# Kernel optimization log

Measured on AMD Instinct MI355X. Metric: run time of the kernel, lower is better.

Reference implementation:

```python
import jax, jax.numpy as jnp
import numpy as np
from jax import lax

NUM_CLASSES = 5  # config['training']['num_classes_per_task']
EMBED_DIM = 64


def _conv(x, w, b, pad):
    y = lax.conv_general_dilated(x, w, (1, 1), [(pad, pad), (pad, pad)],
                                 dimension_numbers=('NCHW', 'OIHW', 'NCHW'))
    return y + b[None, :, None, None]


def _maxpool2(x):
    n, c, h, w = x.shape
    return x.reshape(n, c, h // 2, 2, w // 2, 2).max(axis=(3, 5))


def _lenet(x, c1w, c1b, c2w, c2b, f1w, f1b, f2w, f2b, f3w, f3b):
    h = _maxpool2(jax.nn.relu(_conv(x, c1w, c1b, pad=2)))   # [N,6,14,14]
    h = _maxpool2(jax.nn.relu(_conv(h, c2w, c2b, pad=0)))   # [N,16,5,5]
    h = h.reshape(h.shape[0], -1)                            # [N,400]
    h = jax.nn.relu(h @ f1w.T + f1b)                         # [N,120]
    h = jax.nn.relu(h @ f2w.T + f2b)                         # [N,84]
    return h @ f3w.T + f3b                                   # [N,64]


def setup_inputs() -> dict:
    key = jax.random.key(0)
    ks = jax.random.split(key, 12)
    s = 0.1
    return {
        'x': jax.random.normal(ks[0], (20480, 1, 28, 28), dtype=jnp.float32),
        'c1w': jax.random.normal(ks[1], (6, 1, 5, 5), dtype=jnp.float32) * s,
        'c1b': jnp.zeros((6,), dtype=jnp.float32),
        'c2w': jax.random.normal(ks[2], (16, 6, 5, 5), dtype=jnp.float32) * s,
        'c2b': jnp.zeros((16,), dtype=jnp.float32),
        'f1w': jax.random.normal(ks[3], (120, 400), dtype=jnp.float32) * s,
        'f1b': jnp.zeros((120,), dtype=jnp.float32),
        'f2w': jax.random.normal(ks[4], (84, 120), dtype=jnp.float32) * s,
        'f2b': jnp.zeros((84,), dtype=jnp.float32),
        'f3w': jax.random.normal(ks[5], (EMBED_DIM, 84), dtype=jnp.float32) * s,
        'f3b': jnp.zeros((EMBED_DIM,), dtype=jnp.float32),
    }


def reference(x, c1w, c1b, c2w, c2b, f1w, f1b, f2w, f2b, f3w, f3b):
    emb = _lenet(x, c1w, c1b, c2w, c2b, f1w, f1b, f2w, f2b, f3w, f3b)  # [N,D]
    # Source builds a flat prototypes list of all N*D scalars / num_classes,
    # but only indices 0..D-1 are ever read -> first embedding row / num_classes.
    proto = emb[0] / NUM_CLASSES                     # [D]
    s = jax.nn.softmax(emb, axis=1)                  # softmax over dim 1
    # fun_L(x, p) = sqrt((x-p)^2) = |x-p|
    logits = jnp.abs(s - proto[None, :])             # [N,D]
    batch_size = x.shape[0] // NUM_CLASSES
    return logits.reshape(batch_size, NUM_CLASSES, -1)
```

## Files before the change

kernel.cpp:

```cpp
#include <hip/hip_runtime.h>


__device__ __forceinline__ int xcd_swizzle(int orig, int nwg) {
    int xcd = orig & 7, q = nwg >> 3, r = nwg & 7;
    int base = (xcd < r) ? xcd * (q + 1) : r * (q + 1) + (xcd - r) * q;
    return base + (orig >> 3);
}

__global__ __launch_bounds__(256) void transpose_x(
    const float* __restrict__ x, float* __restrict__ xt, int nc)
{
    __shared__ float t[64][65];
    const int tx = threadIdx.x & 63, ty = threadIdx.x >> 6;
    const int p0 = blockIdx.x * 64, n0 = blockIdx.y * 64;
    #pragma unroll
    for (int rr = 0; rr < 16; ++rr) {
        int nl = rr * 4 + ty;
        int pp = p0 + tx;
        int pr = pp >> 5, pc = pp & 31;
        float v = 0.f;
        if (pr >= 2 && pr < 30 && pc >= 2 && pc < 30)
            v = x[(size_t)(n0 + nl) * 784 + (pr - 2) * 28 + (pc - 2)];
        t[tx][nl] = v;
    }
    __syncthreads();
    #pragma unroll
    for (int rr = 0; rr < 16; ++rr) {
        int pl = rr * 4 + ty;
        xt[(size_t)(p0 + pl) * nc + n0 + tx] = t[pl][tx];
    }
}

__global__ __launch_bounds__(256, 4) void conv1_bt(
    const float* __restrict__ xt, const float* __restrict__ c1w,
    const float* __restrict__ c1b, float* __restrict__ p1t, int nc)
{
    const int newid = xcd_swizzle(blockIdx.x, gridDim.x);
    const int grp = newid / 196, pos = newid - grp * 196;
    const int py = pos / 14, px = pos - py * 14;
    const int ia = grp * 512 + threadIdx.x;
    const int ib = ia + 256;
    const int pbase = (2 * py) * 32 + 2 * px;

    float pa[36], pb[36];
    #pragma unroll
    for (int r = 0; r < 6; ++r)
        #pragma unroll
        for (int cc = 0; cc < 6; ++cc) {
            const float* p = &xt[(size_t)(pbase + r * 32 + cc) * nc];
            pa[r * 6 + cc] = p[ia];
            pb[r * 6 + cc] = p[ib];
        }

    #pragma unroll
    for (int ch = 0; ch < 6; ++ch) {
        float w[25];
        const float* wp = c1w + ch * 25;
        #pragma unroll
        for (int k = 0; k < 25; ++k) w[k] = wp[k];
        float b = c1b[ch];
        float ma = -1e30f, mb = -1e30f;
        #pragma unroll
        for (int dy = 0; dy < 2; ++dy)
        #pragma unroll
        for (int dx = 0; dx < 2; ++dx) {
            float aa = b, ab = b;
            #pragma unroll
            for (int ky = 0; ky < 5; ++ky)
            #pragma unroll
            for (int kx = 0; kx < 5; ++kx) {
                float ww = w[ky * 5 + kx];
                aa += pa[(dy + ky) * 6 + dx + kx] * ww;
                ab += pb[(dy + ky) * 6 + dx + kx] * ww;
            }
            ma = fmaxf(ma, aa); mb = fmaxf(mb, ab);
        }
        float* o = &p1t[(size_t)(ch * 196 + pos) * nc];
        o[ia] = fmaxf(ma, 0.f);
        o[ib] = fmaxf(mb, 0.f);
    }
}

__global__ __launch_bounds__(256, 4) void conv2_bt(
    const float* __restrict__ p1t, const float* __restrict__ c2w,
    const float* __restrict__ c2b, float* __restrict__ ht, int nc)
{
    const int newid = xcd_swizzle(blockIdx.x, gridDim.x);
    const int grp = newid / 25, pos = newid - grp * 25;
    const int qy = pos / 5, qx = pos - qy * 5;
    const int img = grp * 256 + threadIdx.x;
    const int y0 = 2 * qy, x0 = 2 * qx;

    float acc[64];
    #pragma unroll
    for (int i = 0; i < 64; ++i) acc[i] = 0.f;

    #pragma unroll 1
    for (int ci = 0; ci < 6; ++ci) {
        float pa[36];
        #pragma unroll
        for (int r = 0; r < 6; ++r)
            #pragma unroll
            for (int cc = 0; cc < 6; ++cc)
                pa[r * 6 + cc] =
                    p1t[(size_t)(ci * 196 + (y0 + r) * 14 + x0 + cc) * nc + img];
        #pragma unroll
        for (int oc = 0; oc < 16; ++oc) {
            float w[25];
            const float* wp = c2w + (oc * 6 + ci) * 25;
            #pragma unroll
            for (int k = 0; k < 25; ++k) w[k] = wp[k];
            #pragma unroll
            for (int ky = 0; ky < 5; ++ky)
            #pragma unroll
            for (int kx = 0; kx < 5; ++kx) {
                float ww = w[ky * 5 + kx];
                acc[oc*4+0] += pa[ky*6+kx]       * ww;
                acc[oc*4+1] += pa[ky*6+kx+1]     * ww;
                acc[oc*4+2] += pa[(ky+1)*6+kx]   * ww;
                acc[oc*4+3] += pa[(ky+1)*6+kx+1] * ww;
            }
        }
    }
    #pragma unroll
    for (int oc = 0; oc < 16; ++oc) {
        float b = c2b[oc];
        float m = fmaxf(fmaxf(acc[oc*4+0], acc[oc*4+1]),
                        fmaxf(acc[oc*4+2], acc[oc*4+3])) + b;
        ht[(size_t)(oc * 25 + pos) * nc + img] = fmaxf(m, 0.f);
    }
}

__global__ __launch_bounds__(256, 2) void lenet_fc_t(
    const float* __restrict__ ht,
    const float* __restrict__ f1w, const float* __restrict__ f1b,
    const float* __restrict__ f2w, const float* __restrict__ f2b,
    const float* __restrict__ f3w, const float* __restrict__ f3b,
    float* __restrict__ emb, int nc)
{
    __shared__ float wpool[6400];
    __shared__ float a1[32 * 121];
    __shared__ float a2[32 * 85];

    const int tid = threadIdx.x;
    const int n0 = blockIdx.x * 32;
    const int ig = tid & 7;
    const int og = tid >> 3;

    float acc[16];
    #pragma unroll
    for (int j = 0; j < 16; ++j) acc[j] = 0.f;

    for (int kc = 0; kc < 400; kc += 50) {
        __syncthreads();
        for (int i = tid; i < 6000; i += 256) {
            int r = i / 50, c = i - r * 50;
            int rg = r >> 2, rl = r & 3;
            wpool[c * 128 + (((rg ^ (c & 7)) << 2) | rl)] = f1w[r * 400 + kc + c];
        }
        __syncthreads();
        if (og < 30) {
            #pragma unroll 2
            for (int kk = 0; kk < 50; ++kk) {
                const float* hp = &ht[(size_t)(kc + kk) * nc + n0 + ig * 4];
                float h0 = hp[0], h1 = hp[1], h2 = hp[2], h3 = hp[3];
                float4 wv = *(const float4*)&wpool[kk * 128 + ((og ^ (kk & 7)) << 2)];
                acc[0]  += h0 * wv.x; acc[1]  += h0 * wv.y;
                acc[2]  += h0 * wv.z; acc[3]  += h0 * wv.w;
                acc[4]  += h1 * wv.x; acc[5]  += h1 * wv.y;
                acc[6]  += h1 * wv.z; acc[7]  += h1 * wv.w;
                acc[8]  += h2 * wv.x; acc[9]  += h2 * wv.y;
                acc[10] += h2 * wv.z; acc[11] += h2 * wv.w;
                acc[12] += h3 * wv.x; acc[13] += h3 * wv.y;
                acc[14] += h3 * wv.z; acc[15] += h3 * wv.w;
            }
        }
    }
    __syncthreads();
    if (og < 30) {
        #pragma unroll
        for (int j = 0; j < 4; ++j) {
            int o = og * 4 + j;
            float bb = f1b[o];
            a1[(ig * 4 + 0) * 121 + o] = fmaxf(acc[j]      + bb, 0.f);
            a1[(ig * 4 + 1) * 121 + o] = fmaxf(acc[4 + j]  + bb, 0.f);
            a1[(ig * 4 + 2) * 121 + o] = fmaxf(acc[8 + j]  + bb, 0.f);
            a1[(ig * 4 + 3) * 121 + o] = fmaxf(acc[12 + j] + bb, 0.f);
        }
    }
    #pragma unroll
    for (int j = 0; j < 16; ++j) acc[j] = 0.f;

    for (int kc = 0; kc < 120; kc += 60) {
        __syncthreads();
        for (int i = tid; i < 84 * 60; i += 256) {
            int r = i / 60, c = i - r * 60;
            wpool[r * 61 + c] = f2w[r * 120 + kc + c];
        }
        __syncthreads();
        if (og < 21) {
            for (int kk = 0; kk < 60; ++kk) {
                float h0 = a1[(ig * 4 + 0) * 121 + kc + kk];
                float h1 = a1[(ig * 4 + 1) * 121 + kc + kk];
                float h2 = a1[(ig * 4 + 2) * 121 + kc + kk];
                float h3 = a1[(ig * 4 + 3) * 121 + kc + kk];
                #pragma unroll
                for (int j = 0; j < 4; ++j) {
                    float w = wpool[(og * 4 + j) * 61 + kk];
                    acc[j]      += h0 * w;
                    acc[4 + j]  += h1 * w;
                    acc[8 + j]  += h2 * w;
                    acc[12 + j] += h3 * w;
                }
            }
        }
    }
    __syncthreads();
    if (og < 21) {
        #pragma unroll
        for (int j = 0; j < 4; ++j) {
            int o = og * 4 + j;
            float bb = f2b[o];
            a2[(ig * 4 + 0) * 85 + o] = fmaxf(acc[j]      + bb, 0.f);
            a2[(ig * 4 + 1) * 85 + o] = fmaxf(acc[4 + j]  + bb, 0.f);
            a2[(ig * 4 + 2) * 85 + o] = fmaxf(acc[8 + j]  + bb, 0.f);
            a2[(ig * 4 + 3) * 85 + o] = fmaxf(acc[12 + j] + bb, 0.f);
        }
    }
    for (int i = tid; i < 64 * 84; i += 256) {
        int r = i / 84, c = i - r * 84;
        wpool[r * 85 + c] = f3w[i];
    }
    #pragma unroll
    for (int j = 0; j < 16; ++j) acc[j] = 0.f;
    __syncthreads();

    if (og < 16) {
        for (int kk = 0; kk < 84; ++kk) {
            float h0 = a2[(ig * 4 + 0) * 85 + kk];
            float h1 = a2[(ig * 4 + 1) * 85 + kk];
            float h2 = a2[(ig * 4 + 2) * 85 + kk];
            float h3 = a2[(ig * 4 + 3) * 85 + kk];
            #pragma unroll
            for (int j = 0; j < 4; ++j) {
                float w = wpool[(og * 4 + j) * 85 + kk];
                acc[j]      += h0 * w;
                acc[4 + j]  += h1 * w;
                acc[8 + j]  += h2 * w;
                acc[12 + j] += h3 * w;
            }
        }
    }
    __syncthreads();
    if (og < 16) {
        #pragma unroll
        for (int j = 0; j < 4; ++j) {
            int o = og * 4 + j;
            float bb = f3b[o];
            #pragma unroll
            for (int r = 0; r < 4; ++r)
                a1[(ig * 4 + r) * 67 + o] = acc[r * 4 + j] + bb;
        }
    }
    __syncthreads();
    for (int i = tid; i < 2048; i += 256) {
        int row = i >> 6, o = i & 63;
        emb[(size_t)(n0 + row) * 64 + o] = a1[row * 67 + o];
    }
}

__global__ __launch_bounds__(256) void proto_head(
    const float* __restrict__ emb, float* __restrict__ out, int N)
{
    int row  = blockIdx.x * 4 + (threadIdx.x >> 6);
    int lane = threadIdx.x & 63;
    if (row >= N) return;
    float v = emb[(size_t)row * 64 + lane];
    float m = v;
    #pragma unroll
    for (int off = 32; off >= 1; off >>= 1)
        m = fmaxf(m, __shfl_xor(m, off));
    float e = expf(v - m);
    float s = e;
    #pragma unroll
    for (int off = 32; off >= 1; off >>= 1)
        s += __shfl_xor(s, off);
    float sm = e / s;
    float proto = emb[lane] * 0.2f;
    out[(size_t)row * 64 + lane] = fabsf(sm - proto);
}

extern "C" void kernel_launch(void* const* d_in, const int* in_sizes, int n_in,
                              void* d_out, int out_size, void* d_ws, size_t ws_size,
                              hipStream_t stream)
{
    const float* x   = (const float*)d_in[0];
    const float* c1w = (const float*)d_in[1];
    const float* c1b = (const float*)d_in[2];
    const float* c2w = (const float*)d_in[3];
    const float* c2b = (const float*)d_in[4];
    const float* f1w = (const float*)d_in[5];
    const float* f1b = (const float*)d_in[6];
    const float* f2w = (const float*)d_in[7];
    const float* f2b = (const float*)d_in[8];
    const float* f3w = (const float*)d_in[9];
    const float* f3b = (const float*)d_in[10];
    float* out = (float*)d_out;

    const int N = in_sizes[0] / 784;
    float* base = (float*)d_ws;

    int c = 40;
    const int cands[] = {1, 2, 4, 5, 8, 10, 20, 40};
    for (int k = 0; k < 8; ++k) {
        int cd = cands[k];
        if (N % cd) continue;
        int ncq = N / cd;
        if (ncq % 512) continue;
        size_t need = (size_t)8800 * ncq + (size_t)256 * N;
        if (need <= ws_size) { c = cd; break; }
    }
    const int nc = N / c;

    float* xt  = base;
    float* p1t = base + (size_t)1024 * nc;
    float* ht_ = base;
    float* emb = base + (size_t)2200 * nc;

    for (int k = 0; k < c; ++k) {
        int n0 = k * nc;
        transpose_x<<<dim3(16, nc / 64), 256, 0, stream>>>(
            x + (size_t)n0 * 784, xt, nc);
        conv1_bt<<<196 * (nc / 512), 256, 0, stream>>>(
            xt, c1w, c1b, p1t, nc);
        conv2_bt<<<25 * (nc / 256), 256, 0, stream>>>(
            p1t, c2w, c2b, ht_, nc);
        lenet_fc_t<<<nc / 32, 256, 0, stream>>>(
            ht_, f1w, f1b, f2w, f2b, f3w, f3b, emb + (size_t)n0 * 64, nc);
    }
    proto_head<<<(N + 3) / 4, 256, 0, stream>>>(emb, out, N);
}
```

Measured before the change: 324.3 us.

## Split FC stack into transposed per-layer kernels and vectorize conv1 loads

Replaces the fused shared-memory FC kernel with three separate batch-transposed FC kernels (fc1/fc2/fc3). Each thread computes two images with float2 loads and reads weights as uniform scalar loads. Conv1 now uses float2 loads and stores of adjacent images, and conv2 splits its output channels into two passes to cut register pressure, with launch bounds relaxed. The proto head reads the transposed embedding, so each thread does a full-row softmax. In exchange, intermediates make extra global round-trips between kernels and more launches are issued.

```diff
diff --git a/kernel.cpp b/kernel.cpp
--- a/kernel.cpp
+++ b/kernel.cpp
@@ -31,26 +31,23 @@
     }
 }
 
-__global__ __launch_bounds__(256, 4) void conv1_bt(
+__global__ __launch_bounds__(256, 2) void conv1_bt(
     const float* __restrict__ xt, const float* __restrict__ c1w,
     const float* __restrict__ c1b, float* __restrict__ p1t, int nc)
 {
     const int newid = xcd_swizzle(blockIdx.x, gridDim.x);
     const int grp = newid / 196, pos = newid - grp * 196;
     const int py = pos / 14, px = pos - py * 14;
-    const int ia = grp * 512 + threadIdx.x;
-    const int ib = ia + 256;
+    const int img = grp * 512 + threadIdx.x * 2;
     const int pbase = (2 * py) * 32 + 2 * px;
 
-    float pa[36], pb[36];
+    float2 p[36];
     #pragma unroll
     for (int r = 0; r < 6; ++r)
         #pragma unroll
-        for (int cc = 0; cc < 6; ++cc) {
-            const float* p = &xt[(size_t)(pbase + r * 32 + cc) * nc];
-            pa[r * 6 + cc] = p[ia];
-            pb[r * 6 + cc] = p[ib];
-        }
+        for (int cc = 0; cc < 6; ++cc)
+            p[r * 6 + cc] =
+                *(const float2*)&xt[(size_t)(pbase + r * 32 + cc) * nc + img];
 
     #pragma unroll
     for (int ch = 0; ch < 6; ++ch) {
@@ -70,18 +67,18 @@
             #pragma unroll
             for (int kx = 0; kx < 5; ++kx) {
                 float ww = w[ky * 5 + kx];
-                aa += pa[(dy + ky) * 6 + dx + kx] * ww;
-                ab += pb[(dy + ky) * 6 + dx + kx] * ww;
+                float2 pv = p[(dy + ky) * 6 + dx + kx];
+                aa += pv.x * ww;
+                ab += pv.y * ww;
             }
             ma = fmaxf(ma, aa); mb = fmaxf(mb, ab);
         }
-        float* o = &p1t[(size_t)(ch * 196 + pos) * nc];
-        o[ia] = fmaxf(ma, 0.f);
-        o[ib] = fmaxf(mb, 0.f);
-    }
-}
-
-__global__ __launch_bounds__(256, 4) void conv2_bt(
+        float2 o2 = make_float2(fmaxf(ma, 0.f), fmaxf(mb, 0.f));
+        *(float2*)&p1t[(size_t)(ch * 196 + pos) * nc + img] = o2;
+    }
+}
+
+__global__ __launch_bounds__(256, 2) void conv2_bt(
     const float* __restrict__ p1t, const float* __restrict__ c2w,
     const float* __restrict__ c2b, float* __restrict__ ht, int nc)
 {
@@ -91,203 +88,176 @@
     const int img = grp * 256 + threadIdx.x;
     const int y0 = 2 * qy, x0 = 2 * qx;
 
-    float acc[64];
-    #pragma unroll
-    for (int i = 0; i < 64; ++i) acc[i] = 0.f;
-
     #pragma unroll 1
-    for (int ci = 0; ci < 6; ++ci) {
-        float pa[36];
-        #pragma unroll
-        for (int r = 0; r < 6; ++r)
+    for (int pass = 0; pass < 2; ++pass) {
+        float acc[32];
+        #pragma unroll
+        for (int i = 0; i < 32; ++i) acc[i] = 0.f;
+
+        #pragma unroll 1
+        for (int ci = 0; ci < 6; ++ci) {
+            float pa[36];
             #pragma unroll
-            for (int cc = 0; cc < 6; ++cc)
-                pa[r * 6 + cc] =
-                    p1t[(size_t)(ci * 196 + (y0 + r) * 14 + x0 + cc) * nc + img];
-        #pragma unroll
-        for (int oc = 0; oc < 16; ++oc) {
-            float w[25];
-            const float* wp = c2w + (oc * 6 + ci) * 25;
+            for (int r = 0; r < 6; ++r)
+                #pragma unroll
+                for (int cc = 0; cc < 6; ++cc)
+                    pa[r * 6 + cc] =
+                        p1t[(size_t)(ci * 196 + (y0 + r) * 14 + x0 + cc) * nc + img];
             #pragma unroll
-            for (int k = 0; k < 25; ++k) w[k] = wp[k];
-            #pragma unroll
-            for (int ky = 0; ky < 5; ++ky)
-            #pragma unroll
-            for (int kx = 0; kx < 5; ++kx) {
-                float ww = w[ky * 5 + kx];
-                acc[oc*4+0] += pa[ky*6+kx]       * ww;
-                acc[oc*4+1] += pa[ky*6+kx+1]     * ww;
-                acc[oc*4+2] += pa[(ky+1)*6+kx]   * ww;
-                acc[oc*4+3] += pa[(ky+1)*6+kx+1] * ww;
-            }
-        }
-    }
-    #pragma unroll
-    for (int oc = 0; oc < 16; ++oc) {
-        float b = c2b[oc];
-        float m = fmaxf(fmaxf(acc[oc*4+0], acc[oc*4+1]),
-                        fmaxf(acc[oc*4+2], acc[oc*4+3])) + b;
-        ht[(size_t)(oc * 25 + pos) * nc + img] = fmaxf(m, 0.f);
-    }
-}
-
-__global__ __launch_bounds__(256, 2) void lenet_fc_t(
-    const float* __restrict__ ht,
-    const float* __restrict__ f1w, const float* __restrict__ f1b,
-    const float* __restrict__ f2w, const float* __restrict__ f2b,
-    const float* __restrict__ f3w, const float* __restrict__ f3b,
-    float* __restrict__ emb, int nc)
-{
-    __shared__ float wpool[6400];
-    __shared__ float a1[32 * 121];
-    __shared__ float a2[32 * 85];
-
-    const int tid = threadIdx.x;
-    const int n0 = blockIdx.x * 32;
-    const int ig = tid & 7;
-    const int og = tid >> 3;
-
-    float acc[16];
-    #pragma unroll
-    for (int j = 0; j < 16; ++j) acc[j] = 0.f;
-
-    for (int kc = 0; kc < 400; kc += 50) {
-        __syncthreads();
-        for (int i = tid; i < 6000; i += 256) {
-            int r = i / 50, c = i - r * 50;
-            int rg = r >> 2, rl = r & 3;
-            wpool[c * 128 + (((rg ^ (c & 7)) << 2) | rl)] = f1w[r * 400 + kc + c];
-        }
-        __syncthreads();
-        if (og < 30) {
-            #pragma unroll 2
-            for (int kk = 0; kk < 50; ++kk) {
-                const float* hp = &ht[(size_t)(kc + kk) * nc + n0 + ig * 4];
-                float h0 = hp[0], h1 = hp[1], h2 = hp[2], h3 = hp[3];
-                float4 wv = *(const float4*)&wpool[kk * 128 + ((og ^ (kk & 7)) << 2)];
-                acc[0]  += h0 * wv.x; acc[1]  += h0 * wv.y;
-                acc[2]  += h0 * wv.z; acc[3]  += h0 * wv.w;
-                acc[4]  += h1 * wv.x; acc[5]  += h1 * wv.y;
-                acc[6]  += h1 * wv.z; acc[7]  += h1 * wv.w;
-                acc[8]  += h2 * wv.x; acc[9]  += h2 * wv.y;
-                acc[10] += h2 * wv.z; acc[11] += h2 * wv.w;
-                acc[12] += h3 * wv.x; acc[13] += h3 * wv.y;
-                acc[14] += h3 * wv.z; acc[15] += h3 * wv.w;
-            }
-        }
-    }
-    __syncthreads();
-    if (og < 30) {
-        #pragma unroll
-        for (int j = 0; j < 4; ++j) {
-            int o = og * 4 + j;
-            float bb = f1b[o];
-            a1[(ig * 4 + 0) * 121 + o] = fmaxf(acc[j]      + bb, 0.f);
-            a1[(ig * 4 + 1) * 121 + o] = fmaxf(acc[4 + j]  + bb, 0.f);
-            a1[(ig * 4 + 2) * 121 + o] = fmaxf(acc[8 + j]  + bb, 0.f);
-            a1[(ig * 4 + 3) * 121 + o] = fmaxf(acc[12 + j] + bb, 0.f);
-        }
-    }
-    #pragma unroll
-    for (int j = 0; j < 16; ++j) acc[j] = 0.f;
-
-    for (int kc = 0; kc < 120; kc += 60) {
-        __syncthreads();
-        for (int i = tid; i < 84 * 60; i += 256) {
-            int r = i / 60, c = i - r * 60;
-            wpool[r * 61 + c] = f2w[r * 120 + kc + c];
-        }
-        __syncthreads();
-        if (og < 21) {
-            for (int kk = 0; kk < 60; ++kk) {
-                float h0 = a1[(ig * 4 + 0) * 121 + kc + kk];
-                float h1 = a1[(ig * 4 + 1) * 121 + kc + kk];
-                float h2 = a1[(ig * 4 + 2) * 121 + kc + kk];
-                float h3 = a1[(ig * 4 + 3) * 121 + kc + kk];
+            for (int o8 = 0; o8 < 8; ++o8) {
+                float w[25];
+                const float* wp = c2w + ((pass * 8 + o8) * 6 + ci) * 25;
                 #pragma unroll
-                for (int j = 0; j < 4; ++j) {
-                    float w = wpool[(og * 4 + j) * 61 + kk];
-                    acc[j]      += h0 * w;
-                    acc[4 + j]  += h1 * w;
-                    acc[8 + j]  += h2 * w;
-                    acc[12 + j] += h3 * w;
+                for (int k = 0; k < 25; ++k) w[k] = wp[k];
+                #pragma unroll
+                for (int ky = 0; ky < 5; ++ky)
+                #pragma unroll
+                for (int kx = 0; kx < 5; ++kx) {
+                    float ww = w[ky * 5 + kx];
+                    acc[o8*4+0] += pa[ky*6+kx]       * ww;
+                    acc[o8*4+1] += pa[ky*6+kx+1]     * ww;
+                    acc[o8*4+2] += pa[(ky+1)*6+kx]   * ww;
+                    acc[o8*4+3] += pa[(ky+1)*6+kx+1] * ww;
                 }
             }
         }
-    }
-    __syncthreads();
-    if (og < 21) {
-        #pragma unroll
-        for (int j = 0; j < 4; ++j) {
-            int o = og * 4 + j;
-            float bb = f2b[o];
-            a2[(ig * 4 + 0) * 85 + o] = fmaxf(acc[j]      + bb, 0.f);
-            a2[(ig * 4 + 1) * 85 + o] = fmaxf(acc[4 + j]  + bb, 0.f);
-            a2[(ig * 4 + 2) * 85 + o] = fmaxf(acc[8 + j]  + bb, 0.f);
-            a2[(ig * 4 + 3) * 85 + o] = fmaxf(acc[12 + j] + bb, 0.f);
-        }
-    }
-    for (int i = tid; i < 64 * 84; i += 256) {
-        int r = i / 84, c = i - r * 84;
-        wpool[r * 85 + c] = f3w[i];
-    }
-    #pragma unroll
-    for (int j = 0; j < 16; ++j) acc[j] = 0.f;
-    __syncthreads();
-
-    if (og < 16) {
-        for (int kk = 0; kk < 84; ++kk) {
-            float h0 = a2[(ig * 4 + 0) * 85 + kk];
-            float h1 = a2[(ig * 4 + 1) * 85 + kk];
-            float h2 = a2[(ig * 4 + 2) * 85 + kk];
-            float h3 = a2[(ig * 4 + 3) * 85 + kk];
-            #pragma unroll
-            for (int j = 0; j < 4; ++j) {
-                float w = wpool[(og * 4 + j) * 85 + kk];
-                acc[j]      += h0 * w;
-                acc[4 + j]  += h1 * w;
-                acc[8 + j]  += h2 * w;
-                acc[12 + j] += h3 * w;
-            }
-        }
-    }
-    __syncthreads();
-    if (og < 16) {
-        #pragma unroll
-        for (int j = 0; j < 4; ++j) {
-            int o = og * 4 + j;
-            float bb = f3b[o];
-            #pragma unroll
-            for (int r = 0; r < 4; ++r)
-                a1[(ig * 4 + r) * 67 + o] = acc[r * 4 + j] + bb;
-        }
-    }
-    __syncthreads();
-    for (int i = tid; i < 2048; i += 256) {
-        int row = i >> 6, o = i & 63;
-        emb[(size_t)(n0 + row) * 64 + o] = a1[row * 67 + o];
-    }
-}
-
-__global__ __launch_bounds__(256) void proto_head(
-    const float* __restrict__ emb, float* __restrict__ out, int N)
-{
-    int row  = blockIdx.x * 4 + (threadIdx.x >> 6);
-    int lane = threadIdx.x & 63;
-    if (row >= N) return;
-    float v = emb[(size_t)row * 64 + lane];
-    float m = v;
-    #pragma unroll
-    for (int off = 32; off >= 1; off >>= 1)
-        m = fmaxf(m, __shfl_xor(m, off));
-    float e = expf(v - m);
-    float s = e;
-    #pragma unroll
-    for (int off = 32; off >= 1; off >>= 1)
-        s += __shfl_xor(s, off);
-    float sm = e / s;
-    float proto = emb[lane] * 0.2f;
-    out[(size_t)row * 64 + lane] = fabsf(sm - proto);
+        #pragma unroll
+        for (int o8 = 0; o8 < 8; ++o8) {
+            int oc = pass * 8 + o8;
+            float b = c2b[oc];
+            float m = fmaxf(fmaxf(acc[o8*4+0], acc[o8*4+1]),
+                            fmaxf(acc[o8*4+2], acc[o8*4+3])) + b;
+            ht[(size_t)(oc * 25 + pos) * nc + img] = fmaxf(m, 0.f);
+        }
+    }
+}
+
+__global__ __launch_bounds__(256) void fc1_bt(
+    const float* __restrict__ ht, const float* __restrict__ f1w,
+    const float* __restrict__ f1b, float* __restrict__ a1t, int nc)
+{
+    const int newid = xcd_swizzle(blockIdx.x, gridDim.x);
+    const int grp = newid / 15, og = newid - grp * 15;
+    const int img = grp * 512 + threadIdx.x * 2;
+    const float* wb = f1w + og * 8 * 400;
+
+    float2 acc[8];
+    #pragma unroll
+    for (int j = 0; j < 8; ++j) acc[j] = make_float2(0.f, 0.f);
+
+    #pragma unroll 4
+    for (int k = 0; k < 400; ++k) {
+        float2 hv = *(const float2*)&ht[(size_t)k * nc + img];
+        #pragma unroll
+        for (int j = 0; j < 8; ++j) {
+            float w = wb[j * 400 + k];
+            acc[j].x += hv.x * w;
+            acc[j].y += hv.y * w;
+        }
+    }
+    #pragma unroll
+    for (int j = 0; j < 8; ++j) {
+        int o = og * 8 + j;
+        float b = f1b[o];
+        float2 o2 = make_float2(fmaxf(acc[j].x + b, 0.f),
+                                fmaxf(acc[j].y + b, 0.f));
+        *(float2*)&a1t[(size_t)o * nc + img] = o2;
+    }
+}
+
+__global__ __launch_bounds__(256) void fc2_bt(
+    const float* __restrict__ a1t, const float* __restrict__ f2w,
+    const float* __restrict__ f2b, float* __restrict__ a2t, int nc)
+{
+    const int newid = xcd_swizzle(blockIdx.x, gridDim.x);
+    const int grp = newid / 12, og = newid - grp * 12;
+    const int img = grp * 512 + threadIdx.x * 2;
+    const float* wb = f2w + og * 7 * 120;
+
+    float2 acc[7];
+    #pragma unroll
+    for (int j = 0; j < 7; ++j) acc[j] = make_float2(0.f, 0.f);
+
+    #pragma unroll 4
+    for (int k = 0; k < 120; ++k) {
+        float2 hv = *(const float2*)&a1t[(size_t)k * nc + img];
+        #pragma unroll
+        for (int j = 0; j < 7; ++j) {
+            float w = wb[j * 120 + k];
+            acc[j].x += hv.x * w;
+            acc[j].y += hv.y * w;
+        }
+    }
+    #pragma unroll
+    for (int j = 0; j < 7; ++j) {
+        int o = og * 7 + j;
+        float b = f2b[o];
+        float2 o2 = make_float2(fmaxf(acc[j].x + b, 0.f),
+                                fmaxf(acc[j].y + b, 0.f));
+        *(float2*)&a2t[(size_t)o * nc + img] = o2;
+    }
+}
+
+__global__ __launch_bounds__(256) void fc3_bt(
+    const float* __restrict__ a2t, const float* __restrict__ f3w,
+    const float* __restrict__ f3b, float* __restrict__ embt,
+    int nc, int Ntot, int n0)
+{
+    const int newid = xcd_swizzle(blockIdx.x, gridDim.x);
+    const int grp = newid / 8, og = newid - grp * 8;
+    const int limg = grp * 512 + threadIdx.x * 2;
+    const float* wb = f3w + og * 8 * 84;
+
+    float2 acc[8];
+    #pragma unroll
+    for (int j = 0; j < 8; ++j) acc[j] = make_float2(0.f, 0.f);
+
+    #pragma unroll 4
+    for (int k = 0; k < 84; ++k) {
+        float2 hv = *(const float2*)&a2t[(size_t)k * nc + limg];
+        #pragma unroll
+        for (int j = 0; j < 8; ++j) {
+            float w = wb[j * 84 + k];
+            acc[j].x += hv.x * w;
+            acc[j].y += hv.y * w;
+        }
+    }
+    #pragma unroll
+    for (int j = 0; j < 8; ++j) {
+        int o = og * 8 + j;
+        float b = f3b[o];
+        float2 o2 = make_float2(acc[j].x + b, acc[j].y + b);
+        *(float2*)&embt[(size_t)o * Ntot + n0 + limg] = o2;
+    }
+}
+
+__global__ __launch_bounds__(256) void proto_head_t(
+    const float* __restrict__ embt, float* __restrict__ out, int N)
+{
+    const int img = blockIdx.x * 256 + threadIdx.x;
+    float v[64];
+    float m = -1e30f;
+    #pragma unroll
+    for (int o = 0; o < 64; ++o) {
+        v[o] = embt[(size_t)o * N + img];
+        m = fmaxf(m, v[o]);
+    }
+    float s = 0.f;
+    #pragma unroll
+    for (int o = 0; o < 64; ++o) {
+        v[o] = __expf(v[o] - m);
+        s += v[o];
+    }
+    float inv = __frcp_rn(s);
+    #pragma unroll
+    for (int o = 0; o < 64; o += 4) {
+        float4 r;
+        r.x = fabsf(v[o+0] * inv - embt[(size_t)(o+0) * N] * 0.2f);
+        r.y = fabsf(v[o+1] * inv - embt[(size_t)(o+1) * N] * 0.2f);
+        r.z = fabsf(v[o+2] * inv - embt[(size_t)(o+2) * N] * 0.2f);
+        r.w = fabsf(v[o+3] * inv - embt[(size_t)(o+3) * N] * 0.2f);
+        *(float4*)&out[(size_t)img * 64 + o] = r;
+    }
 }
 
 extern "C" void kernel_launch(void* const* d_in, const int* in_sizes, int n_in,
@@ -322,10 +292,12 @@
     }
     const int nc = N / c;
 
-    float* xt  = base;
-    float* p1t = base + (size_t)1024 * nc;
-    float* ht_ = base;
-    float* emb = base + (size_t)2200 * nc;
+    float* xt   = base;
+    float* p1t  = base + (size_t)1024 * nc;
+    float* ht_  = base;
+    float* a1t  = p1t;
+    float* a2t  = p1t + (size_t)120 * nc;
+    float* embt = base + (size_t)2200 * nc;
 
     for (int k = 0; k < c; ++k) {
         int n0 = k * nc;
@@ -335,8 +307,12 @@
             xt, c1w, c1b, p1t, nc);
         conv2_bt<<<25 * (nc / 256), 256, 0, stream>>>(
             p1t, c2w, c2b, ht_, nc);
-        lenet_fc_t<<<nc / 32, 256, 0, stream>>>(
-            ht_, f1w, f1b, f2w, f2b, f3w, f3b, emb + (size_t)n0 * 64, nc);
-    }
-    proto_head<<<(N + 3) / 4, 256, 0, stream>>>(emb, out, N);
-}
+        fc1_bt<<<15 * (nc / 512), 256, 0, stream>>>(
+            ht_, f1w, f1b, a1t, nc);
+        fc2_bt<<<12 * (nc / 512), 256, 0, stream>>>(
+            a1t, f2w, f2b, a2t, nc);
+        fc3_bt<<<8 * (nc / 512), 256, 0, stream>>>(
+            a2t, f3w, f3b, embt, nc, N, n0);
+    }
+    proto_head_t<<<N / 256, 256, 0, stream>>>(embt, out, N);
+}
```

Result: faster. 297.3 us (-8.3%).
